# Kernel tuning notes

Hardware: AMD Instinct MI355X
Metric: run time of the kernel (lower is better)

The kernel has to match this reference:

```python
import jax, jax.numpy as jnp
import numpy as np

HIDDEN = 1024
NHEAD = 16
HEAD_DIM = HIDDEN // NHEAD
B, S = 2, 2048


def setup_inputs() -> dict:
    key = jax.random.key(0)
    ks = jax.random.split(key, 10)
    scale = 1.0 / np.sqrt(HIDDEN)
    inp = {
        "x": jax.random.normal(ks[0], (B, S, HIDDEN), dtype=jnp.float32),
        "mask": jax.random.randint(ks[1], (B, S), 0, 2).astype(bool),
        "Wq": jax.random.normal(ks[2], (HIDDEN, HIDDEN), dtype=jnp.float32) * scale,
        "bq": jnp.zeros((HIDDEN,), dtype=jnp.float32),
        "Wk": jax.random.normal(ks[3], (HIDDEN, HIDDEN), dtype=jnp.float32) * scale,
        "bk": jnp.zeros((HIDDEN,), dtype=jnp.float32),
        "Wv": jax.random.normal(ks[4], (HIDDEN, HIDDEN), dtype=jnp.float32) * scale,
        "bv": jnp.zeros((HIDDEN,), dtype=jnp.float32),
        "Wo": jax.random.normal(ks[5], (HIDDEN, HIDDEN), dtype=jnp.float32) * scale,
        "bo": jnp.zeros((HIDDEN,), dtype=jnp.float32),
    }
    return inp


def reference(x, mask, Wq, bq, Wk, bk, Wv, bv, Wo, bo):
    B_, S_, H = x.shape
    # QKV projections (torch Linear: x @ W.T + b), split into heads -> [B, nhead, S, head_dim]
    def split_heads(t):
        return t.reshape(B_, S_, NHEAD, HEAD_DIM).transpose(0, 2, 1, 3)

    q = split_heads(x @ Wq.T + bq)
    k = split_heads(x @ Wk.T + bk)
    v = split_heads(x @ Wv.T + bv)

    # scaled dot-product scores: [B, nhead, S, S]
    energy = jnp.einsum("bhqd,bhkd->bhqk", q, k) / jnp.sqrt(jnp.float32(HEAD_DIM))

    # combined padding + diagonal-exclusion mask: mask keys where mask[b,k] is True,
    # but never mask the diagonal (self) position
    eye = jnp.eye(S_, dtype=bool)  # [S, S]
    attn_mask = mask[:, None, None, :] & ~eye[None, None, :, :]  # [B, 1, S, S] broadcast over heads
    energy = jnp.where(attn_mask, -jnp.inf, energy)

    attention = jax.nn.softmax(energy, axis=-1)
    out = jnp.einsum("bhqk,bhkd->bhqd", attention, v)  # [B, nhead, S, head_dim]
    out = out.transpose(0, 2, 1, 3).reshape(B_, S_, H)
    return out @ Wo.T + bo
```

## Files before the change

kernel.cpp:

```cpp
#include <hip/hip_runtime.h>

typedef __attribute__((ext_vector_type(8))) short short8;
typedef __attribute__((ext_vector_type(4))) float f32x4;
typedef __attribute__((ext_vector_type(16))) float f32x16;
typedef __attribute__((ext_vector_type(4))) unsigned short ushort4v;

#define HIDDEN 1024
#define NHEAD 16
#define HD 64
#define BATCH 2
#define SEQ 2048
#define MROWS (BATCH * SEQ)
#define QSCALE 0.18033688011112042f

__device__ __forceinline__ unsigned short f2b(float f) {
  union { float f; unsigned u; } v; v.f = f;
  unsigned r = v.u + 0x7fffu + ((v.u >> 16) & 1u);
  return (unsigned short)(r >> 16);
}

__device__ __forceinline__ unsigned cvt_pk_bf16(float lo, float hi) {
  unsigned r;
  asm("v_cvt_pk_bf16_f32 %0, %1, %2" : "=v"(r) : "v"(lo), "v"(hi));
  return r;
}

__device__ __forceinline__ float fexp2(float x) {
#if __has_builtin(__builtin_amdgcn_exp2f)
  return __builtin_amdgcn_exp2f(x);
#else
  return exp2f(x);
#endif
}

__device__ __forceinline__ void gll16(const void* g, void* l) {
  __builtin_amdgcn_global_load_lds(
      (__attribute__((address_space(1))) void*)g,
      (__attribute__((address_space(3))) void*)l, 16, 0, 0);
}

__global__ void prep_kernel(const float* __restrict__ x,
                            const float* __restrict__ Wq,
                            const float* __restrict__ Wk,
                            const float* __restrict__ Wv,
                            const float* __restrict__ Wo,
                            unsigned short* __restrict__ xb,
                            unsigned short* __restrict__ wqb,
                            unsigned short* __restrict__ wkb,
                            unsigned short* __restrict__ wvb,
                            unsigned short* __restrict__ wob) {
  int bid = blockIdx.x;
  const float* src;
  unsigned short* dst;
  int base;
  if (bid < 4096)      { src = x;  dst = xb;  base = bid; }
  else if (bid < 5120) { src = Wq; dst = wqb; base = bid - 4096; }
  else if (bid < 6144) { src = Wk; dst = wkb; base = bid - 5120; }
  else if (bid < 7168) { src = Wv; dst = wvb; base = bid - 6144; }
  else                 { src = Wo; dst = wob; base = bid - 7168; }
  int i = (base * 256 + threadIdx.x) * 4;
  float4 v = *reinterpret_cast<const float4*>(src + i);
  ushort4v o;
  o.x = f2b(v.x); o.y = f2b(v.y); o.z = f2b(v.z); o.w = f2b(v.w);
  *reinterpret_cast<ushort4v*>(dst + i) = o;
}

__global__ void amask_kernel(const int* __restrict__ m, float* __restrict__ am,
                             int n) {
  int i = blockIdx.x * blockDim.x + threadIdx.x;
  if (i < n) am[i] = m[i] ? -1e30f : 0.f;
}

__global__ __launch_bounds__(256) void gemm_qkv_kernel(
    const unsigned short* __restrict__ A,
    const unsigned short* __restrict__ W0,
    const unsigned short* __restrict__ W1,
    const unsigned short* __restrict__ W2,
    const float* __restrict__ c0, const float* __restrict__ c1,
    const float* __restrict__ c2, void* __restrict__ o0,
    void* __restrict__ o1, void* __restrict__ o2) {
  __shared__ __align__(16) unsigned short Al[2][128 * 64];
  __shared__ __align__(16) unsigned short Bl[2][128 * 64];
  const int t = threadIdx.x;
  const int w = t >> 6, l = t & 63;
  const int hi = l >> 4, lo16 = l & 15;
  const int wr = w >> 1, wc = w & 1;
  const int m0 = blockIdx.x * 128;
  const int n0 = blockIdx.y * 128;
  const int K = HIDDEN;

  const int region = n0 >> 10;
  const int n_loc = n0 & 1023;
  const unsigned short* Bsel = region == 0 ? W0 : (region == 1 ? W1 : W2);
  const float* bias = region == 0 ? c0 : (region == 1 ? c1 : c2);

  const int srow = w * 32 + (l >> 3);
  const int schunk = (l & 7) ^ (l >> 3);
  const int rsw = (lo16 & 7);

  const unsigned short* pA[4];
  const unsigned short* pB[4];
#pragma unroll
  for (int i = 0; i < 4; ++i) {
    pA[i] = A + (size_t)(m0 + srow + i * 8) * K + schunk * 8;
    pB[i] = Bsel + (size_t)(n_loc + srow + i * 8) * K + schunk * 8;
  }

  f32x4 acc[4][4];
#pragma unroll
  for (int mi = 0; mi < 4; ++mi)
#pragma unroll
    for (int f = 0; f < 4; ++f) acc[mi][f] = f32x4{0.f, 0.f, 0.f, 0.f};

#pragma unroll
  for (int i = 0; i < 4; ++i) {
    gll16(pA[i], &Al[0][(w * 32 + i * 8) * 64]);
    gll16(pB[i], &Bl[0][(w * 32 + i * 8) * 64]);
    pA[i] += 64; pB[i] += 64;
  }
  __syncthreads();

  auto step = [&](int knext, int BUF) __attribute__((always_inline)) {
    if (knext < K) {
#pragma unroll
      for (int i = 0; i < 4; ++i) {
        gll16(pA[i], &Al[BUF ^ 1][(w * 32 + i * 8) * 64]);
        gll16(pB[i], &Bl[BUF ^ 1][(w * 32 + i * 8) * 64]);
        pA[i] += 64; pB[i] += 64;
      }
    }
#pragma unroll
    for (int kk = 0; kk < 2; ++kk) {
      short8 af[4], bf[4];
#pragma unroll
      for (int mi = 0; mi < 4; ++mi) {
        int row = wr * 64 + mi * 16 + lo16;
        af[mi] = *reinterpret_cast<const short8*>(
            &Al[BUF][row * 64 + (((kk * 4 + hi) ^ rsw) * 8)]);
      }
#pragma unroll
      for (int f = 0; f < 4; ++f) {
        int row = wc * 64 + f * 16 + lo16;
        bf[f] = *reinterpret_cast<const short8*>(
            &Bl[BUF][row * 64 + (((kk * 4 + hi) ^ rsw) * 8)]);
      }
#pragma unroll
      for (int mi = 0; mi < 4; ++mi)
#pragma unroll
        for (int f = 0; f < 4; ++f)
          acc[mi][f] =
              __builtin_amdgcn_mfma_f32_16x16x32_bf16(af[mi], bf[f], acc[mi][f], 0, 0, 0);
    }
    __syncthreads();
  };

  for (int kt = 0; kt < K; kt += 128) {
    step(kt + 64, 0);
    step(kt + 128, 1);
  }

#pragma unroll
  for (int mi = 0; mi < 4; ++mi)
#pragma unroll
    for (int f = 0; f < 4; ++f) {
      int mbase = m0 + wr * 64 + mi * 16 + hi * 4;
      int n_rel = n_loc + wc * 64 + f * 16 + lo16;
      float bv_ = bias[n_rel];
      if (region == 2) {
        int b = mbase >> 11, s = mbase & 2047, d = n_rel & 63, h = n_rel >> 6;
        uint2 pk;
        pk.x = cvt_pk_bf16(acc[mi][f][0] + bv_, acc[mi][f][1] + bv_);
        pk.y = cvt_pk_bf16(acc[mi][f][2] + bv_, acc[mi][f][3] + bv_);
        *reinterpret_cast<uint2*>(
            (unsigned short*)o2 + ((size_t)(b * NHEAD + h) * HD + d) * SEQ + s) = pk;
        continue;
      }
#pragma unroll
      for (int j = 0; j < 4; ++j) {
        float v = acc[mi][f][j] + bv_;
        int mm = mbase + j;
        int b = mm >> 11, s = mm & 2047, h = n_rel >> 6, d = n_rel & 63;
        if (region == 0)
          ((unsigned short*)o0)[((size_t)(b * NHEAD + h) * SEQ + s) * HD + d] =
              f2b(v * QSCALE);
        else
          ((unsigned short*)o1)[((size_t)(b * NHEAD + h) * SEQ + s) * HD + d] =
              f2b(v);
      }
    }
}

__global__ __launch_bounds__(256) void gemm_o_kernel(
    const unsigned short* __restrict__ A, const unsigned short* __restrict__ W0,
    const float* __restrict__ bias, float* __restrict__ out) {
  __shared__ __align__(16) unsigned short Al[2][64 * 64];
  __shared__ __align__(16) unsigned short Bl[2][128 * 64];
  const int t = threadIdx.x;
  const int w = t >> 6, l = t & 63;
  const int hi = l >> 4, lo16 = l & 15;
  const int m0 = blockIdx.x * 64;
  const int n0 = blockIdx.y * 128;
  const int K = HIDDEN;

  const int schunk = (l & 7) ^ (l >> 3);
  const int rsw = (lo16 & 7);

  const unsigned short* pA[2];
#pragma unroll
  for (int i = 0; i < 2; ++i)
    pA[i] = A + (size_t)(m0 + w * 16 + i * 8 + (l >> 3)) * K + schunk * 8;
  const unsigned short* pB[4];
#pragma unroll
  for (int i = 0; i < 4; ++i)
    pB[i] = W0 + (size_t)(n0 + w * 32 + i * 8 + (l >> 3)) * K + schunk * 8;

  f32x4 acc[4][2];
#pragma unroll
  for (int mi = 0; mi < 4; ++mi)
#pragma unroll
    for (int f = 0; f < 2; ++f) acc[mi][f] = f32x4{0.f, 0.f, 0.f, 0.f};

  auto stage = [&](int BUF) __attribute__((always_inline)) {
#pragma unroll
    for (int i = 0; i < 2; ++i) {
      gll16(pA[i], &Al[BUF][(w * 16 + i * 8) * 64]);
      pA[i] += 64;
    }
#pragma unroll
    for (int i = 0; i < 4; ++i) {
      gll16(pB[i], &Bl[BUF][(w * 32 + i * 8) * 64]);
      pB[i] += 64;
    }
  };

  stage(0);
  __syncthreads();

  auto step = [&](int knext, int BUF) __attribute__((always_inline)) {
    if (knext < K) stage(BUF ^ 1);
#pragma unroll
    for (int kk = 0; kk < 2; ++kk) {
      short8 af[4], bf[2];
#pragma unroll
      for (int mi = 0; mi < 4; ++mi)
        af[mi] = *reinterpret_cast<const short8*>(
            &Al[BUF][(mi * 16 + lo16) * 64 + (((kk * 4 + hi) ^ rsw) * 8)]);
#pragma unroll
      for (int f = 0; f < 2; ++f)
        bf[f] = *reinterpret_cast<const short8*>(
            &Bl[BUF][(w * 32 + f * 16 + lo16) * 64 + (((kk * 4 + hi) ^ rsw) * 8)]);
#pragma unroll
      for (int mi = 0; mi < 4; ++mi)
#pragma unroll
        for (int f = 0; f < 2; ++f)
          acc[mi][f] =
              __builtin_amdgcn_mfma_f32_16x16x32_bf16(af[mi], bf[f], acc[mi][f], 0, 0, 0);
    }
    __syncthreads();
  };

  for (int kt = 0; kt < K; kt += 128) {
    step(kt + 64, 0);
    step(kt + 128, 1);
  }

#pragma unroll
  for (int mi = 0; mi < 4; ++mi)
#pragma unroll
    for (int f = 0; f < 2; ++f) {
      int mbase = m0 + mi * 16 + hi * 4;
      int n = n0 + w * 32 + f * 16 + lo16;
      float bv_ = bias[n];
#pragma unroll
      for (int j = 0; j < 4; ++j)
        out[(size_t)(mbase + j) * HIDDEN + n] = acc[mi][f][j] + bv_;
    }
}

__global__ __launch_bounds__(512) void attn_kernel(
    const unsigned short* __restrict__ Q, const unsigned short* __restrict__ Km,
    const unsigned short* __restrict__ Vt, const float* __restrict__ amf,
    unsigned short* __restrict__ O) {
  __shared__ __align__(16) unsigned short KV[3][2][64 * 64];
  __shared__ float SrwS[4][64];
  const int t = threadIdx.x;
  const int w = t >> 6, l = t & 63;
  const int q31 = l & 31, hi32 = l >> 5;
  const int qg = w >> 1, half = w & 1;
  const int nb = ((blockIdx.x & 7) << 6) | (blockIdx.x >> 3);
  const int qt = nb & 15, bh = nb >> 4;
  const int b = bh >> 4, h = bh & 15;
  const int q0w = qt * 128 + qg * 32;
  const int q = q0w + q31;
  const bool diagw = (half == (qg & 1));
  const int dtile = qt * 128 + (qg >> 1) * 64;

  const unsigned short* Qb = Q + (size_t)bh * SEQ * HD;
  const unsigned short* Kb = Km + (size_t)bh * SEQ * HD;
  const unsigned short* Vb = Vt + (size_t)bh * HD * SEQ;
  const float* mb = amf + b * SEQ + half * 32;

  short8 qf[4];
#pragma unroll
  for (int dc = 0; dc < 4; ++dc)
    qf[dc] = *reinterpret_cast<const short8*>(
        Qb + (size_t)q * HD + dc * 16 + hi32 * 8);

  f32x16 o0, o1;
#pragma unroll
  for (int r = 0; r < 16; ++r) { o0[r] = 0.f; o1[r] = 0.f; }
  float srw = 0.f;

  const int srow = w * 8 + (l >> 3);
  const int sc_ = ((l & 7) ^ (l >> 3) ^ (w & 3)) * 8;
  const unsigned short* pK = Kb + (size_t)srow * HD + sc_;
  const unsigned short* pV = Vb + (size_t)srow * SEQ + sc_;

  gll16(pK, &KV[0][0][(w * 8) * 64]);
  gll16(pV, &KV[0][1][(w * 8) * 64]);
  pK += 64 * HD; pV += 64;
  gll16(pK, &KV[1][0][(w * 8) * 64]);
  gll16(pV, &KV[1][1][(w * 8) * 64]);
  pK += 64 * HD; pV += 64;
  asm volatile("s_waitcnt vmcnt(2)" ::: "memory");
  __builtin_amdgcn_s_barrier();
  __builtin_amdgcn_sched_barrier(0);

  const int rk = (q31 & 7) ^ (q31 >> 3);

  auto step = [&](int k0, int BUF, int NBUF, int WAITN) __attribute__((always_inline)) {
    float4 a0[4];
#pragma unroll
    for (int g = 0; g < 4; ++g)
      a0[g] = *reinterpret_cast<const float4*>(mb + k0 + g * 8 + hi32 * 4);

    if (k0 + 128 < SEQ) {
      gll16(pK, &KV[NBUF][0][(w * 8) * 64]);
      gll16(pV, &KV[NBUF][1][(w * 8) * 64]);
      pK += 64 * HD; pV += 64;
    }

    f32x16 s0;
    if (diagw && k0 == dtile) {
      int kb = hi32 * 4;
#pragma unroll
      for (int g = 0; g < 4; ++g) {
        if (kb + g * 8 + 0 == q31) a0[g].x = 0.f;
        if (kb + g * 8 + 1 == q31) a0[g].y = 0.f;
        if (kb + g * 8 + 2 == q31) a0[g].z = 0.f;
        if (kb + g * 8 + 3 == q31) a0[g].w = 0.f;
      }
    }
#pragma unroll
    for (int g = 0; g < 4; ++g) {
      s0[4 * g + 0] = a0[g].x; s0[4 * g + 1] = a0[g].y;
      s0[4 * g + 2] = a0[g].z; s0[4 * g + 3] = a0[g].w;
    }

    __builtin_amdgcn_s_setprio(1);
#pragma unroll
    for (int dc = 0; dc < 4; ++dc) {
      short8 kf = *reinterpret_cast<const short8*>(
          &KV[BUF][0][(half * 32 + q31) * 64 + (((dc * 2 + hi32) ^ rk) * 8)]);
      s0 = __builtin_amdgcn_mfma_f32_32x32x16_bf16(kf, qf[dc], s0, 0, 0, 0);
    }
    __builtin_amdgcn_s_setprio(0);

    float sum = 0.f;
#pragma unroll
    for (int r = 0; r < 16; ++r) {
      float p = fexp2(s0[r]);
      s0[r] = p;
      sum += p;
    }
    {
      unsigned a = __float_as_uint(sum), bsw = a;
      auto rr = __builtin_amdgcn_permlane32_swap(a, bsw, false, false);
      sum = __uint_as_float(rr[0]) + __uint_as_float(rr[1]);
    }
    srw += sum;

    unsigned c[8];
#pragma unroll
    for (int R = 0; R < 4; ++R) {
      c[R * 2 + 0] = cvt_pk_bf16(s0[4 * R + 0], s0[4 * R + 1]);
      c[R * 2 + 1] = cvt_pk_bf16(s0[4 * R + 2], s0[4 * R + 3]);
    }

    short8 pb[2];
#pragma unroll
    for (int sl = 0; sl < 2; ++sl) {
      const int R0 = sl * 2;
      auto r0 = __builtin_amdgcn_permlane32_swap(c[R0 * 2 + 0],
                                                 c[(R0 + 1) * 2 + 0], false, false);
      auto r1 = __builtin_amdgcn_permlane32_swap(c[R0 * 2 + 1],
                                                 c[(R0 + 1) * 2 + 1], false, false);
      union { unsigned u[4]; short8 s8; } pu;
      pu.u[0] = r0[0]; pu.u[1] = r1[0]; pu.u[2] = r0[1]; pu.u[3] = r1[1];
      pb[sl] = pu.s8;
    }

    __builtin_amdgcn_s_setprio(1);
#pragma unroll
    for (int sl = 0; sl < 2; ++sl) {
      int ch = (((half * 2 + sl) * 2 + hi32) ^ rk) * 8;
      short8 vf0 = *reinterpret_cast<const short8*>(&KV[BUF][1][q31 * 64 + ch]);
      short8 vf1 =
          *reinterpret_cast<const short8*>(&KV[BUF][1][(32 + q31) * 64 + ch]);
      o0 = __builtin_amdgcn_mfma_f32_32x32x16_bf16(vf0, pb[sl], o0, 0, 0, 0);
      o1 = __builtin_amdgcn_mfma_f32_32x32x16_bf16(vf1, pb[sl], o1, 0, 0, 0);
    }
    __builtin_amdgcn_s_setprio(0);

    if (WAITN == 2)
      asm volatile("s_waitcnt vmcnt(2)" ::: "memory");
    else
      asm volatile("s_waitcnt vmcnt(0)" ::: "memory");
    __builtin_amdgcn_s_barrier();
    __builtin_amdgcn_sched_barrier(0);
  };

  for (int tt = 0; tt < 30; tt += 3) {
    step(tt * 64, 0, 2, 2);
    step((tt + 1) * 64, 1, 0, 2);
    step((tt + 2) * 64, 2, 1, 2);
  }
  step(30 * 64, 0, 2, 0);
  step(31 * 64, 1, 0, 0);

  float* obuf = (float*)&KV[0][0][0];
  if (half) {
    float* d = obuf + (qg * 64 + l) * 33;
#pragma unroll
    for (int r = 0; r < 16; ++r) { d[r] = o0[r]; d[16 + r] = o1[r]; }
    SrwS[qg][l] = srw;
  }
  __syncthreads();
  if (!half) {
    const float* d = obuf + (qg * 64 + l) * 33;
#pragma unroll
    for (int r = 0; r < 16; ++r) { o0[r] += d[r]; o1[r] += d[16 + r]; }
    srw += SrwS[qg][l];

    float rinv = 1.f / srw;
    unsigned short* Ob = O + (size_t)(b * SEQ + q) * HIDDEN + h * HD;
#pragma unroll
    for (int g = 0; g < 4; ++g) {
      uint2 w0, w1;
      w0.x = cvt_pk_bf16(o0[4 * g + 0] * rinv, o0[4 * g + 1] * rinv);
      w0.y = cvt_pk_bf16(o0[4 * g + 2] * rinv, o0[4 * g + 3] * rinv);
      w1.x = cvt_pk_bf16(o1[4 * g + 0] * rinv, o1[4 * g + 1] * rinv);
      w1.y = cvt_pk_bf16(o1[4 * g + 2] * rinv, o1[4 * g + 3] * rinv);
      *reinterpret_cast<uint2*>(Ob + 8 * g + 4 * hi32) = w0;
      *reinterpret_cast<uint2*>(Ob + 32 + 8 * g + 4 * hi32) = w1;
    }
  }
}

extern "C" void kernel_launch(void* const* d_in, const int* in_sizes, int n_in,
                              void* d_out, int out_size, void* d_ws,
                              size_t ws_size, hipStream_t stream) {
  const float* x = (const float*)d_in[0];
  const int* mask = (const int*)d_in[1];
  const float* Wq = (const float*)d_in[2];
  const float* bq = (const float*)d_in[3];
  const float* Wk = (const float*)d_in[4];
  const float* bk = (const float*)d_in[5];
  const float* Wv = (const float*)d_in[6];
  const float* bv = (const float*)d_in[7];
  const float* Wo = (const float*)d_in[8];
  const float* bo = (const float*)d_in[9];

  char* ws = (char*)d_ws;
  unsigned short* xb  = (unsigned short*)(ws + ((size_t)0 << 20));
  unsigned short* wqb = (unsigned short*)(ws + ((size_t)8 << 20));
  unsigned short* wkb = (unsigned short*)(ws + ((size_t)10 << 20));
  unsigned short* wvb = (unsigned short*)(ws + ((size_t)12 << 20));
  unsigned short* wob = (unsigned short*)(ws + ((size_t)14 << 20));
  unsigned short* qw  = (unsigned short*)(ws + ((size_t)16 << 20));
  unsigned short* kw  = (unsigned short*)(ws + ((size_t)24 << 20));
  unsigned short* vtw = (unsigned short*)(ws + ((size_t)32 << 20));
  unsigned short* ow  = (unsigned short*)(ws + ((size_t)40 << 20));
  float* amf = (float*)(ws + ((size_t)0 << 20));

  prep_kernel<<<8192, 256, 0, stream>>>(x, Wq, Wk, Wv, Wo, xb, wqb, wkb, wvb,
                                        wob);

  gemm_qkv_kernel<<<dim3(MROWS / 128, 3 * HIDDEN / 128), 256, 0, stream>>>(
      xb, wqb, wkb, wvb, bq, bk, bv, qw, kw, vtw);

  amask_kernel<<<MROWS / 256, 256, 0, stream>>>(mask, amf, MROWS);

  attn_kernel<<<512, 512, 0, stream>>>(qw, kw, vtw, amf, ow);

  gemm_o_kernel<<<dim3(MROWS / 64, HIDDEN / 128), 256, 0, stream>>>(
      ow, wob, bo, (float*)d_out);
}
```

Measured before the change: 121.9 us.

## Restructure attention KV pipeline to two-tile steps with four LDS buffers

```diff
diff --git a/kernel.cpp b/kernel.cpp
--- a/kernel.cpp
+++ b/kernel.cpp
@@ -281,7 +281,7 @@
     const unsigned short* __restrict__ Q, const unsigned short* __restrict__ Km,
     const unsigned short* __restrict__ Vt, const float* __restrict__ amf,
     unsigned short* __restrict__ O) {
-  __shared__ __align__(16) unsigned short KV[3][2][64 * 64];
+  __shared__ __align__(16) unsigned short KV[4][2][64 * 64];
   __shared__ float SrwS[4][64];
   const int t = threadIdx.x;
   const int w = t >> 6, l = t & 63;
@@ -316,29 +316,25 @@
   const unsigned short* pK = Kb + (size_t)srow * HD + sc_;
   const unsigned short* pV = Vb + (size_t)srow * SEQ + sc_;
 
-  gll16(pK, &KV[0][0][(w * 8) * 64]);
-  gll16(pV, &KV[0][1][(w * 8) * 64]);
-  pK += 64 * HD; pV += 64;
-  gll16(pK, &KV[1][0][(w * 8) * 64]);
-  gll16(pV, &KV[1][1][(w * 8) * 64]);
-  pK += 64 * HD; pV += 64;
-  asm volatile("s_waitcnt vmcnt(2)" ::: "memory");
+  auto stageT = [&](int BUF) __attribute__((always_inline)) {
+    gll16(pK, &KV[BUF][0][(w * 8) * 64]);
+    gll16(pV, &KV[BUF][1][(w * 8) * 64]);
+    pK += 64 * HD; pV += 64;
+  };
+
+  stageT(0);
+  stageT(1);
+  asm volatile("s_waitcnt vmcnt(0)" ::: "memory");
   __builtin_amdgcn_s_barrier();
   __builtin_amdgcn_sched_barrier(0);
 
   const int rk = (q31 & 7) ^ (q31 >> 3);
 
-  auto step = [&](int k0, int BUF, int NBUF, int WAITN) __attribute__((always_inline)) {
+  auto sub = [&](int k0, int BUF) __attribute__((always_inline)) {
     float4 a0[4];
 #pragma unroll
     for (int g = 0; g < 4; ++g)
       a0[g] = *reinterpret_cast<const float4*>(mb + k0 + g * 8 + hi32 * 4);
-
-    if (k0 + 128 < SEQ) {
-      gll16(pK, &KV[NBUF][0][(w * 8) * 64]);
-      gll16(pV, &KV[NBUF][1][(w * 8) * 64]);
-      pK += 64 * HD; pV += 64;
-    }
 
     f32x16 s0;
     if (diagw && k0 == dtile) {
@@ -411,22 +407,25 @@
       o1 = __builtin_amdgcn_mfma_f32_32x32x16_bf16(vf1, pb[sl], o1, 0, 0, 0);
     }
     __builtin_amdgcn_s_setprio(0);
-
-    if (WAITN == 2)
-      asm volatile("s_waitcnt vmcnt(2)" ::: "memory");
-    else
-      asm volatile("s_waitcnt vmcnt(0)" ::: "memory");
+  };
+
+  auto pairstep = [&](int k0, int B0, int B1, int S0, int S1)
+      __attribute__((always_inline)) {
+    if (k0 + 128 < SEQ) {
+      stageT(S0);
+      stageT(S1);
+    }
+    sub(k0, B0);
+    sub(k0 + 64, B1);
+    asm volatile("s_waitcnt vmcnt(0)" ::: "memory");
     __builtin_amdgcn_s_barrier();
     __builtin_amdgcn_sched_barrier(0);
   };
 
-  for (int tt = 0; tt < 30; tt += 3) {
-    step(tt * 64, 0, 2, 2);
-    step((tt + 1) * 64, 1, 0, 2);
-    step((tt + 2) * 64, 2, 1, 2);
-  }
-  step(30 * 64, 0, 2, 0);
-  step(31 * 64, 1, 0, 0);
+  for (int k0 = 0; k0 < SEQ; k0 += 256) {
+    pairstep(k0, 0, 1, 2, 3);
+    pairstep(k0 + 128, 2, 3, 0, 1);
+  }
 
   float* obuf = (float*)&KV[0][0][0];
   if (half) {
```

Measured after the change: 123.4 us. About the same (+1.2%).
